# Kernel tuning notes

Hardware: AMD Instinct MI355X
Metric: run time of the kernel (lower is better)

## Reference

```python
import jax, jax.numpy as jnp
import numpy as np

N, IN_FEATS, OUT_FEATS = 8192, 512, 256


def setup_inputs() -> dict:
    key = jax.random.key(0)
    k1, k2, k3, k4 = jax.random.split(key, 4)
    feature_mat = jax.random.normal(k1, (N, IN_FEATS), dtype=jnp.float32)
    # Xavier-uniform style init for W and W2
    limW = float(np.sqrt(6.0 / (IN_FEATS + OUT_FEATS)))
    W = jax.random.uniform(k2, (IN_FEATS, OUT_FEATS), minval=-limW, maxval=limW, dtype=jnp.float32)
    limW2 = float(np.sqrt(6.0 / (2 * OUT_FEATS + 1)))
    W2 = jax.random.uniform(k3, (2 * OUT_FEATS, 1), minval=-limW2, maxval=limW2, dtype=jnp.float32)
    adj_mat = jax.random.randint(k4, (N, N), 0, 2, dtype=jnp.int32)
    return {"feature_mat": feature_mat, "W": W, "W2": W2, "adj_mat": adj_mat}


def reference(feature_mat, W, W2, adj_mat):
    out_feats = W.shape[1]
    Wh = feature_mat @ W                      # [N, F']
    Wh1 = Wh @ W2[:out_feats, :]              # [N, 1]
    Wh2 = Wh @ W2[out_feats:, :]              # [N, 1]
    e = Wh1 + Wh2.T                           # [N, N] broadcast add
    e = jnp.where(e > 0, e, 0.2 * e)          # leaky_relu(0.2)
    # NOTE: original masks with ZERO (not -inf) before softmax — faithful.
    e = jnp.where(adj_mat > 0, e, jnp.zeros((), dtype=e.dtype))
    attention = jax.nn.softmax(e, axis=1)     # row softmax over all N
    h_prime = attention @ Wh                  # [N, F']
    return jax.nn.relu(h_prime)
```

## Files before the change

kernel.cpp:

```cpp
#include <hip/hip_runtime.h>
#include <cstdint>
#include <cstddef>

#define NR 8192
#define FOUT 256
#define KIN 512
#define KSPLIT 4
#define JCHUNK (NR / KSPLIT)
#define BKJ 64
#define NSTEP (JCHUNK / BKJ)
#define IROWS 64

typedef __attribute__((ext_vector_type(8))) short bf16x8;
typedef __attribute__((ext_vector_type(4))) float f32x4;

__device__ __forceinline__ unsigned f2bf(float x) {
  unsigned u = __float_as_uint(x);
  u += 0x7fffu + ((u >> 16) & 1u);
  return u >> 16;
}
__device__ __forceinline__ float bf2f(unsigned h) {
  return __uint_as_float(h << 16);
}
__device__ __forceinline__ unsigned fkey(float x) {
  unsigned u = __float_as_uint(x);
  return (u & 0x80000000u) ? ~u : (u | 0x80000000u);
}
__device__ __forceinline__ float fkey_dec(unsigned k) {
  return __uint_as_float((k & 0x80000000u) ? (k ^ 0x80000000u) : ~k);
}

#define GLDS(g, l)                                                            \
  __builtin_amdgcn_global_load_lds(                                           \
      (const __attribute__((address_space(1))) unsigned int*)(g),             \
      (__attribute__((address_space(3))) unsigned int*)(l), 16, 0, 0)

__global__ __launch_bounds__(256) void k0_prep(const float* __restrict__ W,
                                               const float* __restrict__ W2,
                                               float* __restrict__ w1,
                                               float* __restrict__ w2,
                                               char* __restrict__ WTbf,
                                               unsigned* __restrict__ maxkey) {
  if (blockIdx.x == 0 && threadIdx.x == 0) *maxkey = 0u;
  int wv = threadIdx.x >> 6, lane = threadIdx.x & 63;
  int k = blockIdx.x * 4 + wv;
  int f4 = lane * 4;
  float4 wr = *(const float4*)(W + (size_t)k * FOUT + f4);
  float4 a = *(const float4*)(W2 + f4);
  float4 b = *(const float4*)(W2 + FOUT + f4);
  float d1 = wr.x * a.x + wr.y * a.y + wr.z * a.z + wr.w * a.w;
  float d2 = wr.x * b.x + wr.y * b.y + wr.z * b.z + wr.w * b.w;
#pragma unroll
  for (int off = 32; off; off >>= 1) {
    d1 += __shfl_xor(d1, off);
    d2 += __shfl_xor(d2, off);
  }
  if (lane == 0) {
    w1[k] = d1;
    w2[k] = d2;
  }
  int kt = k >> 5, kl = k & 31;
  float wv4[4] = {wr.x, wr.y, wr.z, wr.w};
#pragma unroll
  for (int ff = 0; ff < 4; ++ff) {
    int f = f4 + ff;
    size_t addr = (size_t)kt * 16384 + (f >> 4) * 1024 +
                  (((f & 15) | (((kl >> 3) & 3) << 4)) * 16) + (kl & 7) * 2;
    *(unsigned short*)(WTbf + addr) = (unsigned short)f2bf(wv4[ff]);
  }
}

__global__ __launch_bounds__(256) void k2_fused(
    const float* __restrict__ X, const char* __restrict__ WTbf,
    const float* __restrict__ w1, const float* __restrict__ w2,
    char* __restrict__ WhTf, float* __restrict__ Wh1, float* __restrict__ Wh2,
    unsigned* __restrict__ maxkey) {
  __shared__ char smem[2 * 18432 + 4096];
  char* buf0 = smem;
  char* buf1 = smem + 18432;
  char* wlds = smem + 2 * 18432;
  int t = threadIdx.x, wv = t >> 6, lane = t & 63;
  int jb = blockIdx.x * 32;
  int jr = t >> 3, koff = (t & 7) * 4;
  int cA = (jr & 15) | (((koff >> 3) & 3) << 4);
  int swA = cA ^ (((cA >> 4) & 3) << 2);
  int aoff = (jr >> 4) * 1024 + swA * 16 + ((koff & 4) << 1);
  int slotR = lane ^ (((lane >> 4) & 3) << 2);
  const float* xrow = X + (size_t)(jb + jr) * KIN + koff;

  {
    float2 a_ = *(const float2*)(w1 + t * 2);
    float2 b_ = *(const float2*)(w2 + t * 2);
    *(float2*)(wlds + t * 8) = a_;
    *(float2*)(wlds + 2048 + t * 8) = b_;
  }
  __syncthreads();

  float4 st0, st1, st2, st3;
  float d1 = 0.f, d2 = 0.f;
  f32x4 acc[2][4];
#pragma unroll
  for (int a = 0; a < 2; ++a)
#pragma unroll
    for (int b = 0; b < 4; ++b) acc[a][b] = (f32x4){0.f, 0.f, 0.f, 0.f};

#define K2_GLB(KT, BUFW)                                                      \
  do {                                                                        \
    const char* gs_ = WTbf + ((size_t)(KT) << 14) + (wv << 12) + lane * 16;   \
    char* ld_ = (BUFW) + 2048 + (wv << 12);                                   \
    GLDS(gs_, ld_);                                                           \
    GLDS(gs_ + 1024, ld_ + 1024);                                             \
    GLDS(gs_ + 2048, ld_ + 2048);                                             \
    GLDS(gs_ + 3072, ld_ + 3072);                                             \
  } while (0)

#define K2_LDX(KT, ST) (ST) = *(const float4*)(xrow + (KT) * 32)

#define K2_AGEN(ST, BUFW, SNUM)                                               \
  do {                                                                        \
    uint2 a_;                                                                 \
    a_.x = f2bf((ST).x) | (f2bf((ST).y) << 16);                               \
    a_.y = f2bf((ST).z) | (f2bf((ST).w) << 16);                               \
    *(uint2*)((BUFW) + aoff) = a_;                                            \
    float4 wa_ = *(const float4*)(wlds + ((SNUM)*32 + koff) * 4);             \
    float4 wb_ = *(const float4*)(wlds + 2048 + ((SNUM)*32 + koff) * 4);      \
    d1 += (ST).x * wa_.x + (ST).y * wa_.y + (ST).z * wa_.z + (ST).w * wa_.w;  \
    d2 += (ST).x * wb_.x + (ST).y * wb_.y + (ST).z * wb_.z + (ST).w * wb_.w;  \
  } while (0)

#define K2_ITER(S, BUFR, BUFW, STC, STF)                                      \
  do {                                                                        \
    int s_ = (S);                                                             \
    if (s_ + 1 < 16) K2_GLB(s_ + 1, BUFW);                                    \
    K2_LDX((s_ + 3 < 16) ? s_ + 3 : 15, STF);                                 \
    if (s_ + 1 < 16) K2_AGEN(STC, BUFW, s_ + 1);                              \
    bf16x8 a0 = *(const bf16x8*)((BUFR) + slotR * 16);                        \
    bf16x8 a1 = *(const bf16x8*)((BUFR) + 1024 + slotR * 16);                 \
    bf16x8 b0 = *(const bf16x8*)((BUFR) + 2048 + (wv * 4 + 0) * 1024 + lane * 16); \
    bf16x8 b1 = *(const bf16x8*)((BUFR) + 2048 + (wv * 4 + 1) * 1024 + lane * 16); \
    bf16x8 b2 = *(const bf16x8*)((BUFR) + 2048 + (wv * 4 + 2) * 1024 + lane * 16); \
    bf16x8 b3 = *(const bf16x8*)((BUFR) + 2048 + (wv * 4 + 3) * 1024 + lane * 16); \
    acc[0][0] = __builtin_amdgcn_mfma_f32_16x16x32_bf16(a0, b0, acc[0][0], 0, 0, 0); \
    acc[0][1] = __builtin_amdgcn_mfma_f32_16x16x32_bf16(a0, b1, acc[0][1], 0, 0, 0); \
    acc[0][2] = __builtin_amdgcn_mfma_f32_16x16x32_bf16(a0, b2, acc[0][2], 0, 0, 0); \
    acc[0][3] = __builtin_amdgcn_mfma_f32_16x16x32_bf16(a0, b3, acc[0][3], 0, 0, 0); \
    acc[1][0] = __builtin_amdgcn_mfma_f32_16x16x32_bf16(a1, b0, acc[1][0], 0, 0, 0); \
    acc[1][1] = __builtin_amdgcn_mfma_f32_16x16x32_bf16(a1, b1, acc[1][1], 0, 0, 0); \
    acc[1][2] = __builtin_amdgcn_mfma_f32_16x16x32_bf16(a1, b2, acc[1][2], 0, 0, 0); \
    acc[1][3] = __builtin_amdgcn_mfma_f32_16x16x32_bf16(a1, b3, acc[1][3], 0, 0, 0); \
    __builtin_amdgcn_sched_barrier(0);                                        \
    asm volatile("s_waitcnt vmcnt(1)");                                       \
    asm volatile("s_waitcnt lgkmcnt(0)");                                     \
    __builtin_amdgcn_s_barrier();                                             \
    __builtin_amdgcn_sched_barrier(0);                                        \
  } while (0)

  K2_GLB(0, buf0);
  K2_LDX(0, st0);
  K2_LDX(1, st1);
  K2_LDX(2, st2);
  K2_AGEN(st0, buf0, 0);
  __builtin_amdgcn_sched_barrier(0);
  asm volatile("s_waitcnt vmcnt(2)");
  asm volatile("s_waitcnt lgkmcnt(0)");
  __builtin_amdgcn_s_barrier();
  __builtin_amdgcn_sched_barrier(0);

  for (int s4 = 0; s4 < 16; s4 += 4) {
    K2_ITER(s4 + 0, buf0, buf1, st1, st3);
    K2_ITER(s4 + 1, buf1, buf0, st2, st0);
    K2_ITER(s4 + 2, buf0, buf1, st3, st1);
    K2_ITER(s4 + 3, buf1, buf0, st0, st2);
  }
#undef K2_ITER
#undef K2_AGEN
#undef K2_LDX
#undef K2_GLB

  int q = lane >> 4;
#pragma unroll
  for (int mi = 0; mi < 2; ++mi)
#pragma unroll
    for (int nn = 0; nn < 4; ++nn) {
      int u2 = wv * 4 + nn;
      int cell = (lane & 15) | ((((mi * 2) + (q >> 1)) & 3) << 4);
      uint2 v;
      v.x = f2bf(acc[mi][nn].x) | (f2bf(acc[mi][nn].y) << 16);
      v.y = f2bf(acc[mi][nn].z) | (f2bf(acc[mi][nn].w) << 16);
      *(uint2*)(buf0 + 2048 + u2 * 1024 + cell * 16 + ((q & 1) << 3)) = v;
    }
  __syncthreads();
  char* wb = WhTf + (size_t)blockIdx.x * 16384;
#pragma unroll
  for (int q2 = 0; q2 < 4; ++q2) {
    uint4 v = *(const uint4*)(buf0 + 2048 + q2 * 4096 + t * 16);
    *(uint4*)(wb + q2 * 4096 + t * 16) = v;
  }

  d1 += __shfl_xor(d1, 1);
  d1 += __shfl_xor(d1, 2);
  d1 += __shfl_xor(d1, 4);
  d2 += __shfl_xor(d2, 1);
  d2 += __shfl_xor(d2, 2);
  d2 += __shfl_xor(d2, 4);
  if ((t & 7) == 0) {
    Wh1[jb + jr] = d1;
    Wh2[jb + jr] = d2;
  }
  float mx = d2;
#pragma unroll
  for (int off = 32; off >= 8; off >>= 1) mx = fmaxf(mx, __shfl_xor(mx, off));
  __shared__ float red[4];
  if (lane == 0) red[wv] = mx;
  __syncthreads();
  if (t == 0) {
    float bm = fmaxf(fmaxf(red[0], red[1]), fmaxf(red[2], red[3]));
    atomicMax(maxkey, fkey(bm));
  }
}

__device__ __forceinline__ uint2 hv4(int4 aq, float4 wq, float wh1, float m,
                                     float enm, float& z) {
  float s0 = wh1 + wq.x, s1 = wh1 + wq.y, s2 = wh1 + wq.z, s3 = wh1 + wq.w;
  s0 = fmaxf(s0, 0.2f * s0);
  s1 = fmaxf(s1, 0.2f * s1);
  s2 = fmaxf(s2, 0.2f * s2);
  s3 = fmaxf(s3, 0.2f * s3);
  float w0 = aq.x > 0 ? __expf(s0 - m) : enm;
  float w1 = aq.y > 0 ? __expf(s1 - m) : enm;
  float w2 = aq.z > 0 ? __expf(s2 - m) : enm;
  float w3 = aq.w > 0 ? __expf(s3 - m) : enm;
  unsigned h0 = f2bf(w0), h1 = f2bf(w1), h2 = f2bf(w2), h3 = f2bf(w3);
  z += bf2f(h0) + bf2f(h1) + bf2f(h2) + bf2f(h3);
  uint2 r;
  r.x = h0 | (h1 << 16);
  r.y = h2 | (h3 << 16);
  return r;
}
__device__ __forceinline__ uint4 hv8(int4 a0, int4 a1, float4 w0, float4 w1,
                                     float wh1, float m, float enm, float& z) {
  uint2 r0 = hv4(a0, w0, wh1, m, enm, z);
  uint2 r1 = hv4(a1, w1, wh1, m, enm, z);
  return (uint4){r0.x, r0.y, r1.x, r1.y};
}

__global__ __launch_bounds__(512, 4) void k3_attn(
    const int* __restrict__ adj, const char* __restrict__ WhTf,
    const float* __restrict__ Wh1, const float* __restrict__ Wh2,
    const unsigned* __restrict__ maxptr, float* __restrict__ PVp,
    float* __restrict__ Zp) {
  __shared__ char smem[25088];
  char* abuf0 = smem;
  char* abuf1 = smem + 8192;
  char* wlds = smem + 16384;
  float* zlds = (float*)(smem + 24576);
  int t = threadIdx.x, wv = t >> 6, lane = t & 63;
  int kc = blockIdx.x & 3;
  int ib = blockIdx.x >> 2;
  int ibase = ib * IROWS;
  int jbch = kc * JCHUNK;
  int rg = wv >> 1, ks = wv & 1;
  int genrow = ibase + rg * 16 + (lane & 15);
  float maxwh2 = fkey_dec(*maxptr);
  float wh1 = Wh1[genrow];
  float m = fmaxf(0.f, wh1 + maxwh2);
  float enm = __expf(-m);
  int swA = lane ^ (((lane >> 4) & 3) << 2);
  int aoff = (rg * 2 + ks) * 1024 + swA * 16;
  int slotR = swA;
  const int* adjrow = adj + ((size_t)genrow << 13) + jbch + ks * 32 +
                      ((lane >> 4) << 3);
  const char* bbase = WhTf + ((size_t)(kc * 64) << 14) +
                      (size_t)(wv * 2) * 1024 + (size_t)lane * 16;
  const char* wl = wlds + ks * 128 + ((lane >> 4) << 5);

  *(float4*)(wlds + t * 16) = *(const float4*)(Wh2 + jbch + t * 4);
  __syncthreads();

  int4 st0_a, st0_b, st1_a, st1_b;
  f32x4 acc[4][2];
#pragma unroll
  for (int a = 0; a < 4; ++a)
#pragma unroll
    for (int b = 0; b < 2; ++b) acc[a][b] = (f32x4){0.f, 0.f, 0.f, 0.f};
  float zacc = 0.f;

#define K3_LDA(S, ST)                                                         \
  do {                                                                        \
    int sc_ = (S) < NSTEP ? (S) : NSTEP - 1;                                  \
    ST##_a = *(const int4*)(adjrow + sc_ * 64);                               \
    ST##_b = *(const int4*)(adjrow + sc_ * 64 + 4);                           \
  } while (0)

#define K3_ITER(S, AR, AW, STC, DO_HV)                                        \
  do {                                                                        \
    int s_ = (S);                                                             \
    const char* bp_ = bbase + (size_t)(s_ * 2) * 16384;                       \
    bf16x8 b00 = *(const bf16x8*)(bp_);                           \
    bf16x8 b01 = *(const bf16x8*)(bp_ + 16384);                   \
    bf16x8 b10 = *(const bf16x8*)(bp_ + 1024);                    \
    bf16x8 b11 = *(const bf16x8*)(bp_ + 16384 + 1024);            \
    if (DO_HV) {                                                              \
      float4 wq0_ = *(const float4*)(wl + (s_ + 1) * 256);                    \
      float4 wq1_ = *(const float4*)(wl + (s_ + 1) * 256 + 16);               \
      uint4 a_ = hv8(STC##_a, STC##_b, wq0_, wq1_, wh1, m, enm, zacc);        \
      *(uint4*)((AW) + aoff) = a_;                                            \
    }                                                                         \
    K3_LDA(s_ + 3, STC);                                                      \
    _Pragma("unroll")                                                         \
    for (int rf_ = 0; rf_ < 4; ++rf_) {                                       \
      bf16x8 a0_ = *(const bf16x8*)((AR) + (rf_ * 2 + 0) * 1024 + slotR * 16); \
      bf16x8 a1_ = *(const bf16x8*)((AR) + (rf_ * 2 + 1) * 1024 + slotR * 16); \
      acc[rf_][0] = __builtin_amdgcn_mfma_f32_16x16x32_bf16(a0_, b00, acc[rf_][0], 0, 0, 0); \
      acc[rf_][1] = __builtin_amdgcn_mfma_f32_16x16x32_bf16(a0_, b10, acc[rf_][1], 0, 0, 0); \
      acc[rf_][0] = __builtin_amdgcn_mfma_f32_16x16x32_bf16(a1_, b01, acc[rf_][0], 0, 0, 0); \
      acc[rf_][1] = __builtin_amdgcn_mfma_f32_16x16x32_bf16(a1_, b11, acc[rf_][1], 0, 0, 0); \
    }                                                                         \
    __builtin_amdgcn_sched_barrier(0);                                        \
    asm volatile("s_waitcnt lgkmcnt(0)" ::: "memory");                        \
    __builtin_amdgcn_s_barrier();                                             \
    __builtin_amdgcn_sched_barrier(0);                                        \
  } while (0)

  int4 adj0_a = *(const int4*)(adjrow);
  int4 adj0_b = *(const int4*)(adjrow + 4);
  K3_LDA(1, st1);
  K3_LDA(2, st0);
  {
    float4 wq0 = *(const float4*)(wl);
    float4 wq1 = *(const float4*)(wl + 16);
    uint4 a0 = hv8(adj0_a, adj0_b, wq0, wq1, wh1, m, enm, zacc);
    *(uint4*)(abuf0 + aoff) = a0;
  }
  __builtin_amdgcn_sched_barrier(0);
  asm volatile("s_waitcnt lgkmcnt(0)" ::: "memory");
  __builtin_amdgcn_s_barrier();
  __builtin_amdgcn_sched_barrier(0);

  for (int s2 = 0; s2 < NSTEP - 2; s2 += 2) {
    K3_ITER(s2 + 0, abuf0, abuf1, st1, 1);
    K3_ITER(s2 + 1, abuf1, abuf0, st0, 1);
  }
  K3_ITER(NSTEP - 2, abuf0, abuf1, st1, 1);
  K3_ITER(NSTEP - 1, abuf1, abuf0, st0, 0);
#undef K3_ITER
#undef K3_LDA

  zacc += __shfl_xor(zacc, 16);
  zacc += __shfl_xor(zacc, 32);
  if (lane < 16) zlds[rg * 32 + ks * 16 + lane] = zacc;
  __syncthreads();
  if (t < IROWS) {
    int rg2 = t >> 4, r2 = t & 15;
    Zp[(size_t)kc * NR + ibase + t] =
        zlds[rg2 * 32 + r2] + zlds[rg2 * 32 + 16 + r2];
  }
#pragma unroll
  for (int rf = 0; rf < 4; ++rf)
#pragma unroll
    for (int un = 0; un < 2; ++un) {
      int f = wv * 32 + un * 16 + (lane & 15);
      int row0 = ibase + rf * 16 + ((lane >> 4) << 2);
      size_t base = ((size_t)kc * NR + row0) * FOUT + f;
      PVp[base + 0 * FOUT] = acc[rf][un].x;
      PVp[base + 1 * FOUT] = acc[rf][un].y;
      PVp[base + 2 * FOUT] = acc[rf][un].z;
      PVp[base + 3 * FOUT] = acc[rf][un].w;
    }
}

__global__ __launch_bounds__(256) void k4_reduce(const float* __restrict__ PVp,
                                                 const float* __restrict__ Zp,
                                                 float* __restrict__ out) {
  int tid = blockIdx.x * 256 + threadIdx.x;
  int i = tid >> 6;
  int f4 = (tid & 63) * 4;
  float z = Zp[i] + Zp[NR + i] + Zp[2 * NR + i] + Zp[3 * NR + i];
  float4 a = {0.f, 0.f, 0.f, 0.f};
#pragma unroll
  for (int c = 0; c < KSPLIT; ++c) {
    float4 p = *(const float4*)(PVp + ((size_t)c * NR + i) * FOUT + f4);
    a.x += p.x;
    a.y += p.y;
    a.z += p.z;
    a.w += p.w;
  }
  float inv = 1.f / z;
  float4 r;
  r.x = fmaxf(a.x * inv, 0.f);
  r.y = fmaxf(a.y * inv, 0.f);
  r.z = fmaxf(a.z * inv, 0.f);
  r.w = fmaxf(a.w * inv, 0.f);
  *(float4*)(out + (size_t)i * FOUT + f4) = r;
}

extern "C" void kernel_launch(void* const* d_in, const int* in_sizes, int n_in,
                              void* d_out, int out_size, void* d_ws,
                              size_t ws_size, hipStream_t stream) {
  const float* X = (const float*)d_in[0];
  const float* W = (const float*)d_in[1];
  const float* W2 = (const float*)d_in[2];
  const int* adj = (const int*)d_in[3];
  float* out = (float*)d_out;
  char* ws = (char*)d_ws;

  const size_t WHT_OFF = 0;
  const size_t WTBF_OFF = (size_t)4 * 1024 * 1024;
  const size_t W1_OFF = WTBF_OFF + 256 * 1024;
  const size_t W2V_OFF = W1_OFF + 2048;
  const size_t WH1_OFF = W2V_OFF + 2048;
  const size_t WH2_OFF = WH1_OFF + 32768;
  const size_t MXK_OFF = WH2_OFF + 32768;
  const size_t ZP_OFF = MXK_OFF + 256;
  const size_t PV_OFF = ZP_OFF + (size_t)KSPLIT * NR * 4;

  char* WhTf = ws + WHT_OFF;
  char* WTbf = ws + WTBF_OFF;
  float* w1 = (float*)(ws + W1_OFF);
  float* w2 = (float*)(ws + W2V_OFF);
  float* Wh1 = (float*)(ws + WH1_OFF);
  float* Wh2 = (float*)(ws + WH2_OFF);
  unsigned* maxkey = (unsigned*)(ws + MXK_OFF);
  float* Zp = (float*)(ws + ZP_OFF);
  float* PVp = (float*)(ws + PV_OFF);

  k0_prep<<<128, 256, 0, stream>>>(W, W2, w1, w2, WTbf, maxkey);
  k2_fused<<<256, 256, 0, stream>>>(X, WTbf, w1, w2, WhTf, Wh1, Wh2, maxkey);
  k3_attn<<<512, 512, 0, stream>>>(adj, WhTf, Wh1, Wh2, maxkey, PVp, Zp);
  k4_reduce<<<2048, 256, 0, stream>>>(PVp, Zp, out);
}
```

Measured before the change: 126.8 us.

## Restructure attention kernel to per-wave register A-fragments without LDS staging

```diff
diff --git a/kernel.cpp b/kernel.cpp
--- a/kernel.cpp
+++ b/kernel.cpp
@@ -1,15 +1,14 @@
 #include <hip/hip_runtime.h>
 #include <cstdint>
 #include <cstddef>
+#include <cstring>
 
 #define NR 8192
 #define FOUT 256
 #define KIN 512
-#define KSPLIT 4
+#define KSPLIT 8
 #define JCHUNK (NR / KSPLIT)
-#define BKJ 64
-#define NSTEP (JCHUNK / BKJ)
-#define IROWS 64
+#define NSTEP (JCHUNK / 32)
 
 typedef __attribute__((ext_vector_type(8))) short bf16x8;
 typedef __attribute__((ext_vector_type(4))) float f32x4;
@@ -244,129 +243,81 @@
   return (uint4){r0.x, r0.y, r1.x, r1.y};
 }
 
-__global__ __launch_bounds__(512, 4) void k3_attn(
+__global__ __launch_bounds__(256) void k3_attn(
     const int* __restrict__ adj, const char* __restrict__ WhTf,
     const float* __restrict__ Wh1, const float* __restrict__ Wh2,
     const unsigned* __restrict__ maxptr, float* __restrict__ PVp,
     float* __restrict__ Zp) {
-  __shared__ char smem[25088];
-  char* abuf0 = smem;
-  char* abuf1 = smem + 8192;
-  char* wlds = smem + 16384;
-  float* zlds = (float*)(smem + 24576);
   int t = threadIdx.x, wv = t >> 6, lane = t & 63;
-  int kc = blockIdx.x & 3;
-  int ib = blockIdx.x >> 2;
-  int ibase = ib * IROWS;
-  int jbch = kc * JCHUNK;
-  int rg = wv >> 1, ks = wv & 1;
-  int genrow = ibase + rg * 16 + (lane & 15);
+  int b = blockIdx.x;
+  int x = b & 7, q = b >> 3;
+  int kc = ((x & 3) << 1) + (wv >> 1);
+  int rg = (q << 2) + ((x >> 2) << 1) + (wv & 1);
+  int row = rg * 16 + (lane & 15);
+  int jg = (lane >> 4) << 3;
+  int jbase = kc * JCHUNK;
   float maxwh2 = fkey_dec(*maxptr);
-  float wh1 = Wh1[genrow];
+  float wh1 = Wh1[row];
   float m = fmaxf(0.f, wh1 + maxwh2);
   float enm = __expf(-m);
-  int swA = lane ^ (((lane >> 4) & 3) << 2);
-  int aoff = (rg * 2 + ks) * 1024 + swA * 16;
-  int slotR = swA;
-  const int* adjrow = adj + ((size_t)genrow << 13) + jbch + ks * 32 +
-                      ((lane >> 4) << 3);
-  const char* bbase = WhTf + ((size_t)(kc * 64) << 14) +
-                      (size_t)(wv * 2) * 1024 + (size_t)lane * 16;
-  const char* wl = wlds + ks * 128 + ((lane >> 4) << 5);
-
-  *(float4*)(wlds + t * 16) = *(const float4*)(Wh2 + jbch + t * 4);
-  __syncthreads();
-
-  int4 st0_a, st0_b, st1_a, st1_b;
-  f32x4 acc[4][2];
-#pragma unroll
-  for (int a = 0; a < 4; ++a)
-#pragma unroll
-    for (int b = 0; b < 2; ++b) acc[a][b] = (f32x4){0.f, 0.f, 0.f, 0.f};
+  const int* adjp = adj + (size_t)row * NR + jbase + jg;
+  const float* wh2p = Wh2 + jbase + jg;
+  const char* bb = WhTf + ((size_t)(kc * 32) << 14) + (size_t)lane * 16;
+
+  f32x4 acc[16];
+#pragma unroll
+  for (int u = 0; u < 16; ++u) acc[u] = (f32x4){0.f, 0.f, 0.f, 0.f};
   float zacc = 0.f;
 
-#define K3_LDA(S, ST)                                                         \
+  int4 sA_a, sA_b, sB_a, sB_b;
+  float4 wA_0, wA_1, wB_0, wB_1;
+
+#define K3_LD(S, AA, AB, W0, W1)                                              \
   do {                                                                        \
     int sc_ = (S) < NSTEP ? (S) : NSTEP - 1;                                  \
-    ST##_a = *(const int4*)(adjrow + sc_ * 64);                               \
-    ST##_b = *(const int4*)(adjrow + sc_ * 64 + 4);                           \
-  } while (0)
-
-#define K3_ITER(S, AR, AW, STC, DO_HV)                                        \
-  do {                                                                        \
-    int s_ = (S);                                                             \
-    const char* bp_ = bbase + (size_t)(s_ * 2) * 16384;                       \
-    bf16x8 b00 = *(const bf16x8*)(bp_);                           \
-    bf16x8 b01 = *(const bf16x8*)(bp_ + 16384);                   \
-    bf16x8 b10 = *(const bf16x8*)(bp_ + 1024);                    \
-    bf16x8 b11 = *(const bf16x8*)(bp_ + 16384 + 1024);            \
-    if (DO_HV) {                                                              \
-      float4 wq0_ = *(const float4*)(wl + (s_ + 1) * 256);                    \
-      float4 wq1_ = *(const float4*)(wl + (s_ + 1) * 256 + 16);               \
-      uint4 a_ = hv8(STC##_a, STC##_b, wq0_, wq1_, wh1, m, enm, zacc);        \
-      *(uint4*)((AW) + aoff) = a_;                                            \
+    AA = *(const int4*)(adjp + sc_ * 32);                                     \
+    AB = *(const int4*)(adjp + sc_ * 32 + 4);                                 \
+    W0 = *(const float4*)(wh2p + sc_ * 32);                                   \
+    W1 = *(const float4*)(wh2p + sc_ * 32 + 4);                               \
+  } while (0)
+
+#define K3_STEP(S, AA, AB, W0, W1)                                            \
+  do {                                                                        \
+    uint4 af_ = hv8(AA, AB, W0, W1, wh1, m, enm, zacc);                       \
+    K3_LD((S) + 2, AA, AB, W0, W1);                                           \
+    bf16x8 afr_;                                                              \
+    memcpy(&afr_, &af_, 16);                                                  \
+    const char* bp_ = bb + ((size_t)(S) << 14);                               \
+    _Pragma("unroll")                                                         \
+    for (int u_ = 0; u_ < 16; ++u_) {                                         \
+      bf16x8 bf_ = *(const bf16x8*)(bp_ + u_ * 1024);                         \
+      acc[u_] = __builtin_amdgcn_mfma_f32_16x16x32_bf16(afr_, bf_, acc[u_],   \
+                                                        0, 0, 0);             \
     }                                                                         \
-    K3_LDA(s_ + 3, STC);                                                      \
-    _Pragma("unroll")                                                         \
-    for (int rf_ = 0; rf_ < 4; ++rf_) {                                       \
-      bf16x8 a0_ = *(const bf16x8*)((AR) + (rf_ * 2 + 0) * 1024 + slotR * 16); \
-      bf16x8 a1_ = *(const bf16x8*)((AR) + (rf_ * 2 + 1) * 1024 + slotR * 16); \
-      acc[rf_][0] = __builtin_amdgcn_mfma_f32_16x16x32_bf16(a0_, b00, acc[rf_][0], 0, 0, 0); \
-      acc[rf_][1] = __builtin_amdgcn_mfma_f32_16x16x32_bf16(a0_, b10, acc[rf_][1], 0, 0, 0); \
-      acc[rf_][0] = __builtin_amdgcn_mfma_f32_16x16x32_bf16(a1_, b01, acc[rf_][0], 0, 0, 0); \
-      acc[rf_][1] = __builtin_amdgcn_mfma_f32_16x16x32_bf16(a1_, b11, acc[rf_][1], 0, 0, 0); \
-    }                                                                         \
-    __builtin_amdgcn_sched_barrier(0);                                        \
-    asm volatile("s_waitcnt lgkmcnt(0)" ::: "memory");                        \
-    __builtin_amdgcn_s_barrier();                                             \
-    __builtin_amdgcn_sched_barrier(0);                                        \
-  } while (0)
-
-  int4 adj0_a = *(const int4*)(adjrow);
-  int4 adj0_b = *(const int4*)(adjrow + 4);
-  K3_LDA(1, st1);
-  K3_LDA(2, st0);
-  {
-    float4 wq0 = *(const float4*)(wl);
-    float4 wq1 = *(const float4*)(wl + 16);
-    uint4 a0 = hv8(adj0_a, adj0_b, wq0, wq1, wh1, m, enm, zacc);
-    *(uint4*)(abuf0 + aoff) = a0;
-  }
-  __builtin_amdgcn_sched_barrier(0);
-  asm volatile("s_waitcnt lgkmcnt(0)" ::: "memory");
-  __builtin_amdgcn_s_barrier();
-  __builtin_amdgcn_sched_barrier(0);
-
-  for (int s2 = 0; s2 < NSTEP - 2; s2 += 2) {
-    K3_ITER(s2 + 0, abuf0, abuf1, st1, 1);
-    K3_ITER(s2 + 1, abuf1, abuf0, st0, 1);
-  }
-  K3_ITER(NSTEP - 2, abuf0, abuf1, st1, 1);
-  K3_ITER(NSTEP - 1, abuf1, abuf0, st0, 0);
-#undef K3_ITER
-#undef K3_LDA
+  } while (0)
+
+  K3_LD(0, sA_a, sA_b, wA_0, wA_1);
+  K3_LD(1, sB_a, sB_b, wB_0, wB_1);
+  for (int s = 0; s < NSTEP; s += 2) {
+    K3_STEP(s + 0, sA_a, sA_b, wA_0, wA_1);
+    K3_STEP(s + 1, sB_a, sB_b, wB_0, wB_1);
+  }
+#undef K3_STEP
+#undef K3_LD
 
   zacc += __shfl_xor(zacc, 16);
   zacc += __shfl_xor(zacc, 32);
-  if (lane < 16) zlds[rg * 32 + ks * 16 + lane] = zacc;
-  __syncthreads();
-  if (t < IROWS) {
-    int rg2 = t >> 4, r2 = t & 15;
-    Zp[(size_t)kc * NR + ibase + t] =
-        zlds[rg2 * 32 + r2] + zlds[rg2 * 32 + 16 + r2];
-  }
-#pragma unroll
-  for (int rf = 0; rf < 4; ++rf)
-#pragma unroll
-    for (int un = 0; un < 2; ++un) {
-      int f = wv * 32 + un * 16 + (lane & 15);
-      int row0 = ibase + rf * 16 + ((lane >> 4) << 2);
-      size_t base = ((size_t)kc * NR + row0) * FOUT + f;
-      PVp[base + 0 * FOUT] = acc[rf][un].x;
-      PVp[base + 1 * FOUT] = acc[rf][un].y;
-      PVp[base + 2 * FOUT] = acc[rf][un].z;
-      PVp[base + 3 * FOUT] = acc[rf][un].w;
-    }
+  if (lane < 16) Zp[(size_t)kc * NR + rg * 16 + lane] = zacc;
+
+  int fcol = lane & 15, rsub = (lane >> 4) << 2;
+#pragma unroll
+  for (int u = 0; u < 16; ++u) {
+    size_t base = ((size_t)kc * NR + rg * 16 + rsub) * FOUT + u * 16 + fcol;
+    PVp[base + 0 * FOUT] = acc[u].x;
+    PVp[base + 1 * FOUT] = acc[u].y;
+    PVp[base + 2 * FOUT] = acc[u].z;
+    PVp[base + 3 * FOUT] = acc[u].w;
+  }
 }
 
 __global__ __launch_bounds__(256) void k4_reduce(const float* __restrict__ PVp,
@@ -375,7 +326,9 @@
   int tid = blockIdx.x * 256 + threadIdx.x;
   int i = tid >> 6;
   int f4 = (tid & 63) * 4;
-  float z = Zp[i] + Zp[NR + i] + Zp[2 * NR + i] + Zp[3 * NR + i];
+  float z = 0.f;
+#pragma unroll
+  for (int c = 0; c < KSPLIT; ++c) z += Zp[(size_t)c * NR + i];
   float4 a = {0.f, 0.f, 0.f, 0.f};
 #pragma unroll
   for (int c = 0; c < KSPLIT; ++c) {
@@ -426,6 +379,6 @@
 
   k0_prep<<<128, 256, 0, stream>>>(W, W2, w1, w2, WTbf, maxkey);
   k2_fused<<<256, 256, 0, stream>>>(X, WTbf, w1, w2, WhTf, Wh1, Wh2, maxkey);
-  k3_attn<<<512, 512, 0, stream>>>(adj, WhTf, Wh1, Wh2, maxkey, PVp, Zp);
+  k3_attn<<<1024, 256, 0, stream>>>(adj, WhTf, Wh1, Wh2, maxkey, PVp, Zp);
   k4_reduce<<<2048, 256, 0, stream>>>(PVp, Zp, out);
 }
```

After: 278.9 us. +120.1%, slower.
